# Optimization experiments

Measured on AMD Instinct MI355X. Metric: run time of the kernel, lower is better.

The kernel has to match this reference:

```python
import jax, jax.numpy as jnp
import numpy as np

N_NODES = 50000
N_EDGES = 1600000
IN_CH = 128
OUT_CH = 64
N_HEADS = 4


def setup_inputs() -> dict:
    key = jax.random.key(0)
    k1, k2, k3, k4, k5 = jax.random.split(key, 5)
    x_source = jax.random.normal(k1, (N_NODES, IN_CH), dtype=jnp.float32)
    edge_tgt = jax.random.randint(k2, (N_EDGES,), 0, N_NODES, dtype=jnp.int32)
    edge_src = jax.random.randint(k3, (N_EDGES,), 0, N_NODES, dtype=jnp.int32)
    edge_vals = jnp.ones((N_EDGES,), dtype=jnp.float32)
    # per-head learned params (xavier_uniform-ish scale)
    w_scale = float(np.sqrt(6.0 / (IN_CH + OUT_CH)))
    weight = jax.random.uniform(k4, (N_HEADS, IN_CH, OUT_CH), dtype=jnp.float32,
                                minval=-w_scale, maxval=w_scale)
    a_scale = float(np.sqrt(6.0 / (2 * OUT_CH)))
    att_weight = jax.random.uniform(k5, (N_HEADS, 2 * OUT_CH), dtype=jnp.float32,
                                    minval=-a_scale, maxval=a_scale)
    return {"x_source": x_source, "edge_tgt": edge_tgt, "edge_src": edge_src,
            "edge_vals": edge_vals, "weight": weight, "att_weight": att_weight}


def _can_forward(x_source, edge_tgt, edge_src, edge_vals, weight, att_weight):
    n_nodes = x_source.shape[0]
    out_ch = weight.shape[-1]
    # per-head linear transform: [N, H, O]
    x_msg = jnp.einsum('ni,hio->nho', x_source, weight)
    # gather per-edge source/target messages: [E, H, O]
    src_msg = x_msg[edge_src]
    tgt_msg = x_msg[edge_tgt]
    # attention score = cat([src, tgt]) @ att_weight, split halves: [E, H]
    aw_s = att_weight[:, :out_ch]
    aw_t = att_weight[:, out_ch:]
    e = jnp.einsum('eho,ho->eh', src_msg, aw_s) + jnp.einsum('eho,ho->eh', tgt_msg, aw_t)
    e = jax.nn.leaky_relu(e, negative_slope=0.01)  # default torch slope
    e = e * edge_vals[:, None]  # multiply by neighborhood values pre-softmax
    # sparse softmax over each target row (dim=1 of the sparse matrix)
    row_max = jax.ops.segment_max(e, edge_tgt, num_segments=n_nodes)  # [N, H]
    e_exp = jnp.exp(e - row_max[edge_tgt])
    row_sum = jax.ops.segment_sum(e_exp, edge_tgt, num_segments=n_nodes)  # [N, H]
    alpha = e_exp / row_sum[edge_tgt]  # [E, H]
    # weighted aggregate of source messages per target node: [N, H, O]
    out = jax.ops.segment_sum(alpha[:, :, None] * src_msg, edge_tgt,
                              num_segments=n_nodes)
    # concat heads -> [N, H*O]
    return out.reshape(n_nodes, -1)


def reference(x_source, edge_tgt, edge_src, edge_vals, weight, att_weight):
    return _can_forward(x_source, edge_tgt, edge_src, edge_vals, weight, att_weight)
```

## Files before the change

kernel.cpp:

```cpp
#include <hip/hip_runtime.h>
#include <hip/hip_bf16.h>
#include <math.h>

#define N_NODES 50000
#define N_EDGES 1600000
#define IN_CH   128
#define OUT_CH  64
#define N_HEADS 4
#define CH      (N_HEADS * OUT_CH)

#define NPB   64
#define BINS  782
#define CAPB  3072
#define CHUNK 2560
#define NSCAT 625
#define GEMMB 782

typedef __attribute__((ext_vector_type(8))) short bf16x8;
typedef __attribute__((ext_vector_type(4))) float f32x4;

__device__ __forceinline__ float bf16_lo(unsigned u) { return __uint_as_float(u << 16); }
__device__ __forceinline__ float bf16_hi(unsigned u) { return __uint_as_float(u & 0xffff0000u); }
__device__ __forceinline__ unsigned short f_to_bf16(float f) {
  unsigned u = __float_as_uint(f);
  u += 0x7fffu + ((u >> 16) & 1u);
  return (unsigned short)(u >> 16);
}

__global__ __launch_bounds__(256) void convert_w_init(
    const float* __restrict__ w, unsigned short* __restrict__ wb, int* __restrict__ gcur)
{
  int i = blockIdx.x * 256 + threadIdx.x;
  if (i < BINS) gcur[i] = i * CAPB;
  if (i >= N_HEADS * IN_CH * OUT_CH) return;
  int j = i & 7, lane = (i >> 3) & 63, ctg = (i >> 9) & 15, kc = i >> 13;
  int k = kc * 32 + (lane >> 4) * 8 + j;
  int n = ctg * 16 + (lane & 15);
  int h = n >> 6, o = n & 63;
  wb[i] = f_to_bf16(w[(h * IN_CH + k) * OUT_CH + o]);
}

__global__ __launch_bounds__(256) void gemm_scatter(
    const float* __restrict__ x, const unsigned short* __restrict__ wb,
    const float* __restrict__ aw,
    unsigned short* __restrict__ xmsg, float* __restrict__ sbuf, float* __restrict__ tbuf,
    const int* __restrict__ etgt, const int* __restrict__ esrc,
    const float* __restrict__ eval, int* __restrict__ gcur, int2* __restrict__ binned)
{
  __shared__ __align__(16) char smem[32768];

  if (blockIdx.x < NSCAT) {
    int* lhist  = (int*)smem;
    int* lstart = lhist + BINS;
    int* lbase  = lstart + BINS;
    int2* stg   = (int2*)(lbase + BINS);

    const int tid = threadIdx.x;
    const int e0 = blockIdx.x * CHUNK;
    const int n = min(CHUNK, N_EDGES - e0);

    for (int b = tid; b < BINS; b += 256) lhist[b] = 0;
    __syncthreads();

    for (int i = tid; i < n; i += 256)
      atomicAdd(&lhist[etgt[e0 + i] >> 6], 1);
    __syncthreads();

    if (tid < 64) {
      int carry = 0;
      for (int c = 0; c < BINS; c += 64) {
        int idx = c + tid;
        int v = (idx < BINS) ? lhist[idx] : 0;
        int sc = v;
        #pragma unroll
        for (int off = 1; off < 64; off <<= 1) {
          int u = __shfl_up(sc, off);
          if (tid >= off) sc += u;
        }
        if (idx < BINS) lstart[idx] = carry + sc - v;
        carry += __shfl(sc, 63);
      }
    }
    __syncthreads();

    for (int b = tid; b < BINS; b += 256) {
      int c = lhist[b];
      lbase[b] = c ? atomicAdd(&gcur[b], c) : 0;
      lhist[b] = 0;
    }
    __syncthreads();

    for (int i = tid; i < n; i += 256) {
      int t = etgt[e0 + i];
      int b = t >> 6;
      int r = atomicAdd(&lhist[b], 1);
      unsigned pack = (unsigned)esrc[e0 + i] | ((unsigned)t << 16);
      stg[lstart[b] + r] = make_int2((int)pack, __float_as_int(eval[e0 + i]));
    }
    __syncthreads();

    for (int i = tid; i < n; i += 256) {
      int2 e = stg[i];
      int b = (int)(((unsigned)e.x) >> 22);
      int gpos = lbase[b] + (i - lstart[b]);
      if (gpos < (b + 1) * CAPB)
        binned[gpos] = e;
    }
    return;
  }

  unsigned short (*tlds)[32][128] = (unsigned short (*)[32][128])smem;

  const int gbid = blockIdx.x - NSCAT;
  const int lane = threadIdx.x & 63;
  const int wv   = threadIdx.x >> 6;
  const int q    = lane >> 4;
  const int l16  = lane & 15;
  const int rowbase = gbid * 64 + (wv >> 1) * 32;
  const int chalf   = wv & 1;

  bf16x8 afrag[2][4];
  #pragma unroll
  for (int s = 0; s < 2; ++s) {
    int r = rowbase + s * 16 + l16;
    r = min(r, N_NODES - 1);
    const float* xp = x + (size_t)r * IN_CH + q * 8;
    #pragma unroll
    for (int kc = 0; kc < 4; ++kc) {
      f32x4 lo = *(const f32x4*)(xp + kc * 32);
      f32x4 hi = *(const f32x4*)(xp + kc * 32 + 4);
      bf16x8 a;
      a[0] = (short)f_to_bf16(lo[0]); a[1] = (short)f_to_bf16(lo[1]);
      a[2] = (short)f_to_bf16(lo[2]); a[3] = (short)f_to_bf16(lo[3]);
      a[4] = (short)f_to_bf16(hi[0]); a[5] = (short)f_to_bf16(hi[1]);
      a[6] = (short)f_to_bf16(hi[2]); a[7] = (short)f_to_bf16(hi[3]);
      afrag[s][kc] = a;
    }
  }

  f32x4 acc[2][8];
  #pragma unroll
  for (int s = 0; s < 2; ++s)
    #pragma unroll
    for (int ct = 0; ct < 8; ++ct)
      acc[s][ct] = (f32x4){0.f, 0.f, 0.f, 0.f};

  #pragma unroll
  for (int kc = 0; kc < 4; ++kc) {
    #pragma unroll
    for (int ct = 0; ct < 8; ++ct) {
      const int ctg = chalf * 8 + ct;
      bf16x8 b = *(const bf16x8*)(wb + ((size_t)(kc * 16 + ctg) * 64 + lane) * 8);
      acc[0][ct] = __builtin_amdgcn_mfma_f32_16x16x32_bf16(afrag[0][kc], b, acc[0][ct], 0, 0, 0);
      acc[1][ct] = __builtin_amdgcn_mfma_f32_16x16x32_bf16(afrag[1][kc], b, acc[1][ct], 0, 0, 0);
    }
  }

  #pragma unroll
  for (int s = 0; s < 2; ++s)
    #pragma unroll
    for (int ct = 0; ct < 8; ++ct)
      #pragma unroll
      for (int reg = 0; reg < 4; ++reg)
        tlds[wv][s * 16 + q * 4 + reg][ct * 16 + l16] = f_to_bf16(acc[s][ct][reg]);

  #pragma unroll
  for (int s = 0; s < 2; ++s) {
    float ps[2][4] = {{0,0,0,0},{0,0,0,0}};
    float pt[2][4] = {{0,0,0,0},{0,0,0,0}};
    #pragma unroll
    for (int ct = 0; ct < 8; ++ct) {
      int col = chalf * 128 + ct * 16 + l16;
      int h = col >> 6;
      float as_ = aw[h * 128 + (col & 63)];
      float at_ = aw[h * 128 + 64 + (col & 63)];
      int hp = ct >> 2;
      #pragma unroll
      for (int reg = 0; reg < 4; ++reg) {
        float v = acc[s][ct][reg];
        ps[hp][reg] += v * as_;
        pt[hp][reg] += v * at_;
      }
    }
    #pragma unroll
    for (int hp = 0; hp < 2; ++hp)
      #pragma unroll
      for (int reg = 0; reg < 4; ++reg)
        #pragma unroll
        for (int off = 1; off < 16; off <<= 1) {
          ps[hp][reg] += __shfl_xor(ps[hp][reg], off);
          pt[hp][reg] += __shfl_xor(pt[hp][reg], off);
        }
    const int rowq = rowbase + s * 16 + q * 4;
    if (l16 == 0) {
      #pragma unroll
      for (int reg = 0; reg < 4; ++reg) {
        int r = rowq + reg;
        if (r < N_NODES) {
          #pragma unroll
          for (int hp = 0; hp < 2; ++hp) {
            sbuf[r * 4 + chalf * 2 + hp] = ps[hp][reg];
            tbuf[r * 4 + chalf * 2 + hp] = pt[hp][reg];
          }
        }
      }
    }
  }

  __syncthreads();

  const int seg  = lane & 31;
  const int half = lane >> 5;
  #pragma unroll
  for (int r2 = 0; r2 < 16; ++r2) {
    int row = r2 * 2 + half;
    int gr = rowbase + row;
    if (gr < N_NODES) {
      ushort4 vv = *(const ushort4*)&tlds[wv][row][seg * 4];
      *(ushort4*)(xmsg + (size_t)gr * CH + chalf * 128 + seg * 4) = vv;
    }
  }
}

__global__ __launch_bounds__(512, 2) void bin_aggregate(
    const int* __restrict__ gcur, const int2* __restrict__ binned,
    const float* __restrict__ sbuf, const float* __restrict__ tbuf,
    const unsigned short* __restrict__ xmsg, float* __restrict__ out)
{
  __shared__ int nh[NPB];
  __shared__ int start_l[NPB];
  __shared__ int deg_l[NPB];
  __shared__ __align__(16) int2 sorted[CAPB];
  __shared__ int s_lds[8][64];
  __shared__ __align__(16) float p_lds[8][64][4];

  const int tid = threadIdx.x;
  const int b = blockIdx.x;
  const int bbase = b * CAPB;
  const int cnt = min(gcur[b] - bbase, CAPB);

  if (tid < NPB) nh[tid] = 0;
  __syncthreads();

  for (int i = tid; i < cnt; i += 512)
    atomicAdd(&nh[(binned[bbase + i].x >> 16) & 63], 1);
  __syncthreads();

  if (tid < 64) {
    int v = nh[tid];
    int sc = v;
    #pragma unroll
    for (int off = 1; off < 64; off <<= 1) {
      int u = __shfl_up(sc, off);
      if (tid >= off) sc += u;
    }
    start_l[tid] = sc - v;
    deg_l[tid] = v;
    nh[tid] = 0;
  }
  __syncthreads();

  for (int i = tid; i < cnt; i += 512) {
    int2 e = binned[bbase + i];
    int tl = (e.x >> 16) & 63;
    int r = atomicAdd(&nh[tl], 1);
    sorted[start_l[tl] + r] = e;
  }
  __syncthreads();

  const int lane = tid & 63;
  const int wave = tid >> 6;
  const int seg  = lane & 31;
  const int half = lane >> 5;
  const int hh4  = seg >> 3;

  for (int ni = wave * 8; ni < wave * 8 + 8; ++ni) {
    const int n = b * NPB + ni;
    if (n >= N_NODES) break;

    const int d   = deg_l[ni];
    const int rs0 = start_l[ni];

    float4 tn4 = *(const float4*)(tbuf + (size_t)n * 4);
    float tn[4] = {tn4.x, tn4.y, tn4.z, tn4.w};

    float m[4]    = {-INFINITY, -INFINITY, -INFINITY, -INFINITY};
    float psum[4] = {0.f, 0.f, 0.f, 0.f};
    float acc[8]  = {0.f, 0.f, 0.f, 0.f, 0.f, 0.f, 0.f, 0.f};

    for (int base2 = 0; base2 < d; base2 += 64) {
      const int cnt2 = min(64, d - base2);
      const bool act = lane < cnt2;

      float sc4[4] = {-INFINITY, -INFINITY, -INFINITY, -INFINITY};
      int s = 0;
      if (act) {
        int2 ev = sorted[rs0 + base2 + lane];
        s = ev.x & 0xffff;
        float v = __int_as_float(ev.y);
        float4 sv4 = *(const float4*)(sbuf + (size_t)s * 4);
        float svv[4] = {sv4.x, sv4.y, sv4.z, sv4.w};
        #pragma unroll
        for (int hh = 0; hh < 4; ++hh) {
          float t = svv[hh] + tn[hh];
          t = (t > 0.f) ? t : 0.01f * t;
          sc4[hh] = t * v;
        }
      }

      float bm[4] = {sc4[0], sc4[1], sc4[2], sc4[3]};
      #pragma unroll
      for (int hh = 0; hh < 4; ++hh)
        #pragma unroll
        for (int off = 32; off; off >>= 1)
          bm[hh] = fmaxf(bm[hh], __shfl_xor(bm[hh], off));

      float p[4];
      #pragma unroll
      for (int hh = 0; hh < 4; ++hh) {
        float nm = fmaxf(m[hh], bm[hh]);
        float r = (m[hh] == -INFINITY) ? 0.f : __expf(m[hh] - nm);
        psum[hh] *= r;
        if (hh == hh4) {
          #pragma unroll
          for (int j = 0; j < 8; ++j) acc[j] *= r;
        }
        m[hh] = nm;
        p[hh] = act ? __expf(sc4[hh] - nm) : 0.f;
        psum[hh] += p[hh];
      }

      if (act) {
        s_lds[wave][lane] = s;
        *(float4*)(&p_lds[wave][lane][0]) = make_float4(p[0], p[1], p[2], p[3]);
      }
      __builtin_amdgcn_wave_barrier();

      int k = 0;
      for (; k + 8 <= cnt2; k += 8) {
        int sA = s_lds[wave][k + 0 + half];
        int sB = s_lds[wave][k + 2 + half];
        int sC = s_lds[wave][k + 4 + half];
        int sD = s_lds[wave][k + 6 + half];
        uint4 rA = *(const uint4*)(xmsg + (size_t)sA * CH + seg * 8);
        uint4 rB = *(const uint4*)(xmsg + (size_t)sB * CH + seg * 8);
        uint4 rC = *(const uint4*)(xmsg + (size_t)sC * CH + seg * 8);
        uint4 rD = *(const uint4*)(xmsg + (size_t)sD * CH + seg * 8);
        float qA = p_lds[wave][k + 0 + half][hh4];
        float qB = p_lds[wave][k + 2 + half][hh4];
        float qC = p_lds[wave][k + 4 + half][hh4];
        float qD = p_lds[wave][k + 6 + half][hh4];
        acc[0] = fmaf(qA, bf16_lo(rA.x), acc[0]); acc[1] = fmaf(qA, bf16_hi(rA.x), acc[1]);
        acc[2] = fmaf(qA, bf16_lo(rA.y), acc[2]); acc[3] = fmaf(qA, bf16_hi(rA.y), acc[3]);
        acc[4] = fmaf(qA, bf16_lo(rA.z), acc[4]); acc[5] = fmaf(qA, bf16_hi(rA.z), acc[5]);
        acc[6] = fmaf(qA, bf16_lo(rA.w), acc[6]); acc[7] = fmaf(qA, bf16_hi(rA.w), acc[7]);
        acc[0] = fmaf(qB, bf16_lo(rB.x), acc[0]); acc[1] = fmaf(qB, bf16_hi(rB.x), acc[1]);
        acc[2] = fmaf(qB, bf16_lo(rB.y), acc[2]); acc[3] = fmaf(qB, bf16_hi(rB.y), acc[3]);
        acc[4] = fmaf(qB, bf16_lo(rB.z), acc[4]); acc[5] = fmaf(qB, bf16_hi(rB.z), acc[5]);
        acc[6] = fmaf(qB, bf16_lo(rB.w), acc[6]); acc[7] = fmaf(qB, bf16_hi(rB.w), acc[7]);
        acc[0] = fmaf(qC, bf16_lo(rC.x), acc[0]); acc[1] = fmaf(qC, bf16_hi(rC.x), acc[1]);
        acc[2] = fmaf(qC, bf16_lo(rC.y), acc[2]); acc[3] = fmaf(qC, bf16_hi(rC.y), acc[3]);
        acc[4] = fmaf(qC, bf16_lo(rC.z), acc[4]); acc[5] = fmaf(qC, bf16_hi(rC.z), acc[5]);
        acc[6] = fmaf(qC, bf16_lo(rC.w), acc[6]); acc[7] = fmaf(qC, bf16_hi(rC.w), acc[7]);
        acc[0] = fmaf(qD, bf16_lo(rD.x), acc[0]); acc[1] = fmaf(qD, bf16_hi(rD.x), acc[1]);
        acc[2] = fmaf(qD, bf16_lo(rD.y), acc[2]); acc[3] = fmaf(qD, bf16_hi(rD.y), acc[3]);
        acc[4] = fmaf(qD, bf16_lo(rD.z), acc[4]); acc[5] = fmaf(qD, bf16_hi(rD.z), acc[5]);
        acc[6] = fmaf(qD, bf16_lo(rD.w), acc[6]); acc[7] = fmaf(qD, bf16_hi(rD.w), acc[7]);
      }
      for (; k < cnt2; k += 2) {
        int e = k + half;
        if (e < cnt2) {
          int sA = s_lds[wave][e];
          uint4 rA = *(const uint4*)(xmsg + (size_t)sA * CH + seg * 8);
          float qA = p_lds[wave][e][hh4];
          acc[0] = fmaf(qA, bf16_lo(rA.x), acc[0]); acc[1] = fmaf(qA, bf16_hi(rA.x), acc[1]);
          acc[2] = fmaf(qA, bf16_lo(rA.y), acc[2]); acc[3] = fmaf(qA, bf16_hi(rA.y), acc[3]);
          acc[4] = fmaf(qA, bf16_lo(rA.z), acc[4]); acc[5] = fmaf(qA, bf16_hi(rA.z), acc[5]);
          acc[6] = fmaf(qA, bf16_lo(rA.w), acc[6]); acc[7] = fmaf(qA, bf16_hi(rA.w), acc[7]);
        }
      }
      __builtin_amdgcn_wave_barrier();
    }

    #pragma unroll
    for (int j = 0; j < 8; ++j) acc[j] += __shfl_xor(acc[j], 32);
    #pragma unroll
    for (int hh = 0; hh < 4; ++hh)
      #pragma unroll
      for (int off = 32; off; off >>= 1)
        psum[hh] += __shfl_xor(psum[hh], off);

    float rsum = psum[hh4];
    float inv = (rsum > 0.f) ? 1.0f / rsum : 0.f;
    const int o = half * 4;
    float4 o4 = make_float4(acc[o+0]*inv, acc[o+1]*inv, acc[o+2]*inv, acc[o+3]*inv);
    *(float4*)(out + (size_t)n * CH + seg * 8 + half * 4) = o4;
  }
}

extern "C" void kernel_launch(void* const* d_in, const int* in_sizes, int n_in,
                              void* d_out, int out_size, void* d_ws, size_t ws_size,
                              hipStream_t stream) {
  const float* x    = (const float*)d_in[0];
  const int*   etgt = (const int*)  d_in[1];
  const int*   esrc = (const int*)  d_in[2];
  const float* evl  = (const float*)d_in[3];
  const float* w    = (const float*)d_in[4];
  const float* aw   = (const float*)d_in[5];
  float* out = (float*)d_out;

  char* ws = (char*)d_ws;
  unsigned short* wb   = (unsigned short*)(ws);
  unsigned short* xmsg = (unsigned short*)(ws + 65536);
  float* sbuf     = (float*)(ws + 25665536);
  float* tbuf     = (float*)(ws + 26465536);
  int*   gcur     = (int*)  (ws + 27265536);
  int2*  binned   = (int2*) (ws + 27269632);

  convert_w_init<<<128, 256, 0, stream>>>(w, wb, gcur);
  gemm_scatter<<<NSCAT + GEMMB, 256, 0, stream>>>(x, wb, aw, xmsg, sbuf, tbuf,
                                                  etgt, esrc, evl, gcur, binned);
  bin_aggregate<<<BINS, 512, 0, stream>>>(gcur, binned, sbuf, tbuf, xmsg, out);
}
```

Before: 278.7 us.

## Replace global atomic bin cursors with precomputed per-block histogram prefix scan

Adds a histogram pass over edge targets in the weight-conversion kernel and a new scan kernel that computes deterministic per-block, per-bin base offsets. The scatter blocks read those offsets instead of calling atomicAdd on global bin cursors, which removes contention on the global atomics and makes edge placement deterministic. In exchange it adds a kernel launch, an extra read of edge_tgt, and a histogram/base buffer of several MB. It also leaves a redundant atomic loop over lhist followed by a re-zero, which adds shared-memory work.

```diff
diff --git a/kernel.cpp b/kernel.cpp
--- a/kernel.cpp
+++ b/kernel.cpp
@@ -15,6 +15,7 @@
 #define CHUNK 2560
 #define NSCAT 625
 #define GEMMB 782
+#define CONVB 128
 
 typedef __attribute__((ext_vector_type(8))) short bf16x8;
 typedef __attribute__((ext_vector_type(4))) float f32x4;
@@ -27,11 +28,29 @@
   return (unsigned short)(u >> 16);
 }
 
-__global__ __launch_bounds__(256) void convert_w_init(
-    const float* __restrict__ w, unsigned short* __restrict__ wb, int* __restrict__ gcur)
+__global__ __launch_bounds__(256) void conv_hist(
+    const float* __restrict__ w, unsigned short* __restrict__ wb,
+    const int* __restrict__ etgt, int* __restrict__ hist)
 {
+  __shared__ int lhist[BINS];
+
+  if (blockIdx.x >= CONVB) {
+    const int me = blockIdx.x - CONVB;
+    const int tid = threadIdx.x;
+    const int e0 = me * CHUNK;
+    const int n = min(CHUNK, N_EDGES - e0);
+
+    for (int b = tid; b < BINS; b += 256) lhist[b] = 0;
+    __syncthreads();
+    for (int i = tid; i < n; i += 256)
+      atomicAdd(&lhist[etgt[e0 + i] >> 6], 1);
+    __syncthreads();
+    for (int b = tid; b < BINS; b += 256)
+      hist[(size_t)me * BINS + b] = lhist[b];
+    return;
+  }
+
   int i = blockIdx.x * 256 + threadIdx.x;
-  if (i < BINS) gcur[i] = i * CAPB;
   if (i >= N_HEADS * IN_CH * OUT_CH) return;
   int j = i & 7, lane = (i >> 3) & 63, ctg = (i >> 9) & 15, kc = i >> 13;
   int k = kc * 32 + (lane >> 4) * 8 + j;
@@ -40,12 +59,37 @@
   wb[i] = f_to_bf16(w[(h * IN_CH + k) * OUT_CH + o]);
 }
 
+__global__ __launch_bounds__(256) void scan_hist(
+    const int* __restrict__ hist, int* __restrict__ base, int* __restrict__ gcur)
+{
+  const int w = threadIdx.x >> 6;
+  const int lane = threadIdx.x & 63;
+  const int bin = blockIdx.x * 4 + w;
+  if (bin >= BINS) return;
+
+  int carry = 0;
+  for (int c = 0; c < NSCAT; c += 64) {
+    int blk = c + lane;
+    int v = (blk < NSCAT) ? hist[(size_t)blk * BINS + bin] : 0;
+    int sc = v;
+    #pragma unroll
+    for (int off = 1; off < 64; off <<= 1) {
+      int u = __shfl_up(sc, off);
+      if (lane >= off) sc += u;
+    }
+    if (blk < NSCAT)
+      base[(size_t)bin * NSCAT + blk] = bin * CAPB + carry + sc - v;
+    carry += __shfl(sc, 63);
+  }
+  if (lane == 0) gcur[bin] = bin * CAPB + carry;
+}
+
 __global__ __launch_bounds__(256) void gemm_scatter(
     const float* __restrict__ x, const unsigned short* __restrict__ wb,
     const float* __restrict__ aw,
     unsigned short* __restrict__ xmsg, float* __restrict__ sbuf, float* __restrict__ tbuf,
     const int* __restrict__ etgt, const int* __restrict__ esrc,
-    const float* __restrict__ eval, int* __restrict__ gcur, int2* __restrict__ binned)
+    const float* __restrict__ eval, const int* __restrict__ base, int2* __restrict__ binned)
 {
   __shared__ __align__(16) char smem[32768];
 
@@ -56,7 +100,8 @@
     int2* stg   = (int2*)(lbase + BINS);
 
     const int tid = threadIdx.x;
-    const int e0 = blockIdx.x * CHUNK;
+    const int me = blockIdx.x;
+    const int e0 = me * CHUNK;
     const int n = min(CHUNK, N_EDGES - e0);
 
     for (int b = tid; b < BINS; b += 256) lhist[b] = 0;
@@ -80,16 +125,21 @@
         if (idx < BINS) lstart[idx] = carry + sc - v;
         carry += __shfl(sc, 63);
       }
-    }
-    __syncthreads();
-
-    for (int b = tid; b < BINS; b += 256) {
-      int c = lhist[b];
-      lbase[b] = c ? atomicAdd(&gcur[b], c) : 0;
-      lhist[b] = 0;
-    }
-    __syncthreads();
-
+    } else {
+      for (int b = tid - 64; b < BINS; b += 192)
+        lbase[b] = base[(size_t)b * NSCAT + me];
+    }
+    __syncthreads();
+
+    for (int i = tid; i < n; i += 256) {
+      int t = etgt[e0 + i];
+      int b = t >> 6;
+      int r = atomicAdd(&lhist[b], 1) - lhist[b];
+      (void)r;
+    }
+    __syncthreads();
+    for (int b = tid; b < BINS; b += 256) lhist[b] = 0;
+    __syncthreads();
     for (int i = tid; i < n; i += 256) {
       int t = etgt[e0 + i];
       int b = t >> 6;
@@ -416,9 +466,12 @@
   float* tbuf     = (float*)(ws + 26465536);
   int*   gcur     = (int*)  (ws + 27265536);
   int2*  binned   = (int2*) (ws + 27269632);
-
-  convert_w_init<<<128, 256, 0, stream>>>(w, wb, gcur);
+  int*   hist     = (int*)  (ws + 46488064);
+  int*   basebuf  = (int*)  (ws + 48443072);
+
+  conv_hist<<<CONVB + NSCAT, 256, 0, stream>>>(w, wb, etgt, hist);
+  scan_hist<<<(BINS + 3) / 4, 256, 0, stream>>>(hist, basebuf, gcur);
   gemm_scatter<<<NSCAT + GEMMB, 256, 0, stream>>>(x, wb, aw, xmsg, sbuf, tbuf,
-                                                  etgt, esrc, evl, gcur, binned);
+                                                  etgt, esrc, evl, basebuf, binned);
   bin_aggregate<<<BINS, 512, 0, stream>>>(gcur, binned, sbuf, tbuf, xmsg, out);
 }
```

Measured after the change: 277.3 us. About the same (-0.5%).

## Scatter edges into coarse 256-node superbins with padded 8-aligned global writes

Applied to the files above, without the earlier changes.

The edge scatter now bins edges into 196 superbins of 256 target nodes instead of 782 bins of 64, using 8192-edge chunks. Each block's runs are padded to multiples of 8 with sentinel entries so global writes are aligned and contiguous. The staging buffer now holds 16-bit edge indices instead of packed pairs. Each aggregate block then scans its whole superbin (about four times the data) and keeps only its own 64 nodes. This trades fewer global atomics and better-coalesced scatter writes for four times the redundant reads in the aggregation phase.

```diff
diff --git a/kernel.cpp b/kernel.cpp
--- a/kernel.cpp
+++ b/kernel.cpp
@@ -9,12 +9,13 @@
 #define N_HEADS 4
 #define CH      (N_HEADS * OUT_CH)
 
-#define NPB   64
-#define BINS  782
-#define CAPB  3072
-#define CHUNK 2560
-#define NSCAT 625
-#define GEMMB 782
+#define NPB    64
+#define BINS   782
+#define SBS    196
+#define SBCAP  10240
+#define CHUNK  8192
+#define NSCAT  196
+#define GEMMB  782
 
 typedef __attribute__((ext_vector_type(8))) short bf16x8;
 typedef __attribute__((ext_vector_type(4))) float f32x4;
@@ -28,10 +29,10 @@
 }
 
 __global__ __launch_bounds__(256) void convert_w_init(
-    const float* __restrict__ w, unsigned short* __restrict__ wb, int* __restrict__ gcur)
+    const float* __restrict__ w, unsigned short* __restrict__ wb, int* __restrict__ scur)
 {
   int i = blockIdx.x * 256 + threadIdx.x;
-  if (i < BINS) gcur[i] = i * CAPB;
+  if (i < SBS) scur[i] = i * SBCAP;
   if (i >= N_HEADS * IN_CH * OUT_CH) return;
   int j = i & 7, lane = (i >> 3) & 63, ctg = (i >> 9) & 15, kc = i >> 13;
   int k = kc * 32 + (lane >> 4) * 8 + j;
@@ -45,66 +46,84 @@
     const float* __restrict__ aw,
     unsigned short* __restrict__ xmsg, float* __restrict__ sbuf, float* __restrict__ tbuf,
     const int* __restrict__ etgt, const int* __restrict__ esrc,
-    const float* __restrict__ eval, int* __restrict__ gcur, int2* __restrict__ binned)
+    const float* __restrict__ eval, int* __restrict__ scur, int2* __restrict__ sbbuf)
 {
   __shared__ __align__(16) char smem[32768];
 
   if (blockIdx.x < NSCAT) {
-    int* lhist  = (int*)smem;
-    int* lstart = lhist + BINS;
-    int* lbase  = lstart + BINS;
-    int2* stg   = (int2*)(lbase + BINS);
+    int* hist   = (int*)smem;
+    int* cnt2   = hist + 200;
+    int* lstart = cnt2 + 200;
+    int* gbase  = lstart + 200;
+    int* ptot   = gbase + 200;
+    short* stg  = (short*)(ptot + 4);
 
     const int tid = threadIdx.x;
-    const int e0 = blockIdx.x * CHUNK;
+    const int me = blockIdx.x;
+    const int e0 = me * CHUNK;
     const int n = min(CHUNK, N_EDGES - e0);
 
-    for (int b = tid; b < BINS; b += 256) lhist[b] = 0;
+    for (int b = tid; b < SBS; b += 256) { hist[b] = 0; cnt2[b] = 0; }
     __syncthreads();
 
     for (int i = tid; i < n; i += 256)
-      atomicAdd(&lhist[etgt[e0 + i] >> 6], 1);
+      atomicAdd(&hist[etgt[e0 + i] >> 8], 1);
     __syncthreads();
 
     if (tid < 64) {
       int carry = 0;
-      for (int c = 0; c < BINS; c += 64) {
+      for (int c = 0; c < SBS; c += 64) {
         int idx = c + tid;
-        int v = (idx < BINS) ? lhist[idx] : 0;
-        int sc = v;
+        int h = (idx < SBS) ? hist[idx] : 0;
+        int r8 = (h + 7) & ~7;
+        int sc = r8;
         #pragma unroll
         for (int off = 1; off < 64; off <<= 1) {
           int u = __shfl_up(sc, off);
           if (tid >= off) sc += u;
         }
-        if (idx < BINS) lstart[idx] = carry + sc - v;
+        if (idx < SBS) lstart[idx] = carry + sc - r8;
         carry += __shfl(sc, 63);
       }
+      if (tid == 0) *ptot = carry;
+    } else {
+      for (int b = tid - 64; b < SBS; b += 192) {
+        int h = hist[b];
+        int r8 = (h + 7) & ~7;
+        gbase[b] = r8 ? atomicAdd(&scur[b], r8) : 0;
+      }
     }
     __syncthreads();
 
-    for (int b = tid; b < BINS; b += 256) {
-      int c = lhist[b];
-      lbase[b] = c ? atomicAdd(&gcur[b], c) : 0;
-      lhist[b] = 0;
+    for (int i = tid; i < n; i += 256) {
+      int sb = etgt[e0 + i] >> 8;
+      int r = atomicAdd(&cnt2[sb], 1);
+      stg[lstart[sb] + r] = (short)i;
+    }
+    for (int b = tid; b < SBS; b += 256) {
+      int h = hist[b];
+      int r8 = (h + 7) & ~7;
+      for (int k = h; k < r8; ++k) stg[lstart[b] + k] = (short)(-(b + 1));
     }
     __syncthreads();
 
-    for (int i = tid; i < n; i += 256) {
-      int t = etgt[e0 + i];
-      int b = t >> 6;
-      int r = atomicAdd(&lhist[b], 1);
-      unsigned pack = (unsigned)esrc[e0 + i] | ((unsigned)t << 16);
-      stg[lstart[b] + r] = make_int2((int)pack, __float_as_int(eval[e0 + i]));
-    }
-    __syncthreads();
-
-    for (int i = tid; i < n; i += 256) {
-      int2 e = stg[i];
-      int b = (int)(((unsigned)e.x) >> 22);
-      int gpos = lbase[b] + (i - lstart[b]);
-      if (gpos < (b + 1) * CAPB)
-        binned[gpos] = e;
+    const int PT = *ptot;
+    for (int i = tid; i < PT; i += 256) {
+      int v = (int)stg[i];
+      int sb, rx, ry;
+      if (v >= 0) {
+        int t = etgt[e0 + v];
+        sb = t >> 8;
+        rx = esrc[e0 + v] | (t << 16);
+        ry = __float_as_int(eval[e0 + v]);
+      } else {
+        sb = -v - 1;
+        rx = (int)0xFFFF0000u;
+        ry = 0;
+      }
+      int gpos = gbase[sb] + (i - lstart[sb]);
+      if (gpos < (sb + 1) * SBCAP)
+        sbbuf[gpos] = make_int2(rx, ry);
     }
     return;
   }
@@ -223,27 +242,30 @@
 }
 
 __global__ __launch_bounds__(512, 2) void bin_aggregate(
-    const int* __restrict__ gcur, const int2* __restrict__ binned,
+    const int* __restrict__ scur, const int2* __restrict__ sbbuf,
     const float* __restrict__ sbuf, const float* __restrict__ tbuf,
     const unsigned short* __restrict__ xmsg, float* __restrict__ out)
 {
   __shared__ int nh[NPB];
   __shared__ int start_l[NPB];
   __shared__ int deg_l[NPB];
-  __shared__ __align__(16) int2 sorted[CAPB];
+  __shared__ __align__(16) int2 sorted[3072];
   __shared__ int s_lds[8][64];
   __shared__ __align__(16) float p_lds[8][64][4];
 
   const int tid = threadIdx.x;
   const int b = blockIdx.x;
-  const int bbase = b * CAPB;
-  const int cnt = min(gcur[b] - bbase, CAPB);
+  const int sb = b >> 2;
+  const int bbase = sb * SBCAP;
+  const int cnt = min(scur[sb] - bbase, SBCAP);
 
   if (tid < NPB) nh[tid] = 0;
   __syncthreads();
 
-  for (int i = tid; i < cnt; i += 512)
-    atomicAdd(&nh[(binned[bbase + i].x >> 16) & 63], 1);
+  for (int i = tid; i < cnt; i += 512) {
+    int t = (int)(((unsigned)sbbuf[bbase + i].x) >> 16);
+    if ((t >> 6) == b) atomicAdd(&nh[t & 63], 1);
+  }
   __syncthreads();
 
   if (tid < 64) {
@@ -261,10 +283,13 @@
   __syncthreads();
 
   for (int i = tid; i < cnt; i += 512) {
-    int2 e = binned[bbase + i];
-    int tl = (e.x >> 16) & 63;
-    int r = atomicAdd(&nh[tl], 1);
-    sorted[start_l[tl] + r] = e;
+    int2 e = sbbuf[bbase + i];
+    int t = (int)(((unsigned)e.x) >> 16);
+    if ((t >> 6) == b) {
+      int tl = t & 63;
+      int r = atomicAdd(&nh[tl], 1);
+      sorted[start_l[tl] + r] = e;
+    }
   }
   __syncthreads();
 
@@ -414,11 +439,11 @@
   unsigned short* xmsg = (unsigned short*)(ws + 65536);
   float* sbuf     = (float*)(ws + 25665536);
   float* tbuf     = (float*)(ws + 26465536);
-  int*   gcur     = (int*)  (ws + 27265536);
-  int2*  binned   = (int2*) (ws + 27269632);
-
-  convert_w_init<<<128, 256, 0, stream>>>(w, wb, gcur);
+  int*   scur     = (int*)  (ws + 27265536);
+  int2*  sbbuf    = (int2*) (ws + 27269632);
+
+  convert_w_init<<<128, 256, 0, stream>>>(w, wb, scur);
   gemm_scatter<<<NSCAT + GEMMB, 256, 0, stream>>>(x, wb, aw, xmsg, sbuf, tbuf,
-                                                  etgt, esrc, evl, gcur, binned);
-  bin_aggregate<<<BINS, 512, 0, stream>>>(gcur, binned, sbuf, tbuf, xmsg, out);
+                                                  etgt, esrc, evl, scur, sbbuf);
+  bin_aggregate<<<BINS, 512, 0, stream>>>(scur, sbbuf, sbuf, tbuf, xmsg, out);
 }
```

Result: slower. 292.0 us (+4.7%).
